# Kernel optimization log

Measured on AMD Instinct MI355X. Metric: run time of the kernel, lower is better.

## Reference

```python
import jax, jax.numpy as jnp
import numpy as np

D_MODEL, D_STATE, B, S = 1024, 64, 8, 2048


def setup_inputs() -> dict:
    key = jax.random.key(0)
    ks = jax.random.split(key, 14)
    inp = {"x": jax.random.normal(ks[0], (B, S, D_MODEL), jnp.float32)}
    names = ["cog", "beh", "env", "delta", "Bp", "Cp"]
    for i, n in enumerate(names):
        inp[f"W_{n}"] = jax.random.normal(ks[1 + 2 * i], (D_STATE, D_MODEL), jnp.float32) / np.sqrt(D_MODEL)
        inp[f"b_{n}"] = jnp.zeros((D_STATE,), jnp.float32)
    # torch init is log(|randn|+1e-4); we use strictly-negative A_log so the
    # length-2048 multiplicative recurrence stays finite (A_log is a learned
    # parameter, so its value is free; the math of forward is unchanged).
    inp["A_log"] = -jnp.abs(jax.random.normal(ks[13], (D_STATE, D_STATE), jnp.float32)) - 0.1
    return inp


def reference(x, W_cog, b_cog, W_beh, b_beh, W_env, b_env,
              W_delta, b_delta, W_Bp, b_Bp, W_Cp, b_Cp, A_log):
    # gating terms (computed in the source but never used downstream)
    A_t = (jax.nn.sigmoid(x @ W_cog.T + b_cog)
           * jax.nn.sigmoid(x @ W_beh.T + b_beh)
           * jax.nn.sigmoid(x @ W_env.T + b_env))
    del A_t

    delta = jax.nn.softplus(x @ W_delta.T + b_delta)   # [B,S,N]
    Bt = x @ W_Bp.T + b_Bp                             # [B,S,N]
    Ct = x @ W_Cp.T + b_Cp                             # [B,S,N]
    u = Bt * x[:, :, :D_STATE]                         # [B,S,N]

    # Faithful to torch broadcasting: after step 0 the carried state h is
    # [B,N,N] with h[b,i,j] = exp(A_log[i,j]*delta[b,t,i]) * h_prev[b,i,j] + u[b,t,j]
    def step(h, td):
        d, u_t, c_t = td                               # each [B,N]
        A = jnp.exp(A_log[None, :, :] * d[:, :, None]) # [B,N,N]
        h = A * h + u_t[:, None, :]
        y = jnp.einsum('bj,bij->bi', c_t, h)           # [B,N]
        return h, y

    h0 = jnp.zeros((x.shape[0], D_STATE, D_STATE), x.dtype)
    _, ys = jax.lax.scan(
        step, h0,
        (delta.transpose(1, 0, 2), u.transpose(1, 0, 2), Ct.transpose(1, 0, 2)))
    # torch stacks y_t of shape [B,1,N] along dim=1 -> [B,S,1,N]
    return ys.transpose(1, 0, 2)[:, :, None, :]
```

## Files before the change

kernel.cpp:

```cpp
#include <hip/hip_runtime.h>
#include <math.h>

#define DM   1024
#define DS   64
#define BATCH 8
#define SEQ  2048
#define CL   32
#define NC   64

typedef __bf16 bf16x8 __attribute__((ext_vector_type(8)));
typedef float  f32x4  __attribute__((ext_vector_type(4)));

#if __has_builtin(__builtin_amdgcn_exp2f)
#define EXP2(v) __builtin_amdgcn_exp2f(v)
#else
#define EXP2(v) __expf(0.69314718056f * (v))
#endif

#define LBAR() do {                                                           \
    asm volatile("s_waitcnt lgkmcnt(0)" ::: "memory");                        \
    __builtin_amdgcn_s_barrier();                                             \
    asm volatile("" ::: "memory");                                            \
} while (0)

__global__ __launch_bounds__(256) void wconv_kernel(
    const float* __restrict__ Wd, const float* __restrict__ Wb,
    const float* __restrict__ Wc, __bf16* __restrict__ Wp)
{
    int idx = blockIdx.x * 256 + threadIdx.x;
    int k  = idx & 1023;
    int n  = idx >> 10;
    const float* W = (n < 64) ? Wd : (n < 128 ? Wb : Wc);
    float v = W[(size_t)(n & 63) * DM + k];
    int kt = k >> 5, kk = k & 31;
    Wp[((size_t)kt * 192 + n) * 32 + kk] = (__bf16)v;
}

__global__ __launch_bounds__(256, 2) void projp1_full(
    const float* __restrict__ x, const __bf16* __restrict__ Wp,
    const float* __restrict__ bd, const float* __restrict__ bb,
    const float* __restrict__ bc, const float* __restrict__ A_log,
    float* __restrict__ delta_g, float* __restrict__ u_g,
    float* __restrict__ ct_g,
    float* __restrict__ E, float* __restrict__ Dsum)
{
    __shared__ __bf16 sA[4][32 * 72];
    __shared__ float  s_d[CL * 64];
    __shared__ float  s_u[CL * 64];

    const int tid  = threadIdx.x;
    const int row0 = blockIdx.x * 32;

    const int lane = tid & 63, wv = tid >> 6;
    const int l15  = lane & 15, quad = lane >> 4;
    const int nbase = wv * 48;

    const int am = tid >> 3;
    const int ak = tid & 7;
    const float* xga = x + (size_t)(row0 + am) * DM + ak * 8;

    const __bf16* wpb = Wp + (nbase + l15) * 32 + quad * 8;

    f32x4 acc[2][3];
    #pragma unroll
    for (int mt = 0; mt < 2; ++mt)
        #pragma unroll
        for (int nt = 0; nt < 3; ++nt)
            acc[mt][nt] = (f32x4){0.f, 0.f, 0.f, 0.f};

    float4 areg[4];
    bf16x8 bA[6], bB[6];

    #define LOADA2(pp) do {                                                   \
        areg[0] = *(const float4*)(xga + (pp) * 128);                         \
        areg[1] = *(const float4*)(xga + (pp) * 128 + 4);                     \
        areg[2] = *(const float4*)(xga + (pp) * 128 + 64);                    \
        areg[3] = *(const float4*)(xga + (pp) * 128 + 68);                    \
    } while (0)
    #define STAGEA2(be, bo) do {                                              \
        bf16x8 h0 = {(__bf16)areg[0].x, (__bf16)areg[0].y,                    \
                     (__bf16)areg[0].z, (__bf16)areg[0].w,                    \
                     (__bf16)areg[1].x, (__bf16)areg[1].y,                    \
                     (__bf16)areg[1].z, (__bf16)areg[1].w};                   \
        *(bf16x8*)&sA[be][am * 72 + ak * 8] = h0;                             \
        bf16x8 h1 = {(__bf16)areg[2].x, (__bf16)areg[2].y,                    \
                     (__bf16)areg[2].z, (__bf16)areg[2].w,                    \
                     (__bf16)areg[3].x, (__bf16)areg[3].y,                    \
                     (__bf16)areg[3].z, (__bf16)areg[3].w};                   \
        *(bf16x8*)&sA[bo][am * 72 + ak * 8] = h1;                             \
    } while (0)
    #define LOADBF(dst, kb) do {                                              \
        const __bf16* wb_ = wpb + (size_t)(kb) * 12288;                       \
        dst[0] = *(const bf16x8*)(wb_);                                       \
        dst[1] = *(const bf16x8*)(wb_ + 512);                                 \
        dst[2] = *(const bf16x8*)(wb_ + 1024);                                \
        dst[3] = *(const bf16x8*)(wb_ + 6144);                                \
        dst[4] = *(const bf16x8*)(wb_ + 6656);                                \
        dst[5] = *(const bf16x8*)(wb_ + 7168);                                \
    } while (0)
    #define COMPUTE(bi, bfr) do {                                             \
        _Pragma("unroll")                                                     \
        for (int s = 0; s < 2; ++s) {                                         \
            bf16x8 af0 = *(const bf16x8*)                                     \
                &sA[bi][(l15) * 72 + s * 32 + quad * 8];                      \
            bf16x8 af1 = *(const bf16x8*)                                     \
                &sA[bi][(16 + l15) * 72 + s * 32 + quad * 8];                 \
            _Pragma("unroll")                                                 \
            for (int nt = 0; nt < 3; ++nt) {                                  \
                acc[0][nt] = __builtin_amdgcn_mfma_f32_16x16x32_bf16(         \
                    af0, bfr[s * 3 + nt], acc[0][nt], 0, 0, 0);               \
                acc[1][nt] = __builtin_amdgcn_mfma_f32_16x16x32_bf16(         \
                    af1, bfr[s * 3 + nt], acc[1][nt], 0, 0, 0);               \
            }                                                                 \
        }                                                                     \
    } while (0)

    LOADA2(0);
    STAGEA2(0, 1);
    LOADA2(1);
    LOADBF(bA, 0);
    LBAR();

    for (int p = 0; p < 8; ++p) {
        const int pe = (p & 1) * 2, po = pe + 1;
        LOADBF(bB, 2 * p + 1);
        COMPUTE(pe, bA);
        if (p < 7) STAGEA2(pe ^ 2, po ^ 2);
        if (p < 6) LOADA2(p + 2);
        if (p < 7) LOADBF(bA, 2 * p + 2);
        COMPUTE(po, bB);
        LBAR();
    }
    #undef LOADA2
    #undef STAGEA2
    #undef LOADBF
    #undef COMPUTE

    #pragma unroll
    for (int nt = 0; nt < 3; ++nt) {
        int gn  = nbase + nt * 16 + l15;
        int mat = (nbase + nt * 16) >> 6;
        int col = gn & 63;
        float bias = (mat == 0) ? bd[col] : (mat == 1 ? bb[col] : bc[col]);
        #pragma unroll
        for (int mt = 0; mt < 2; ++mt) {
            #pragma unroll
            for (int r = 0; r < 4; ++r) {
                int tl = mt * 16 + quad * 4 + r;
                int m  = row0 + tl;
                float v = acc[mt][nt][r] + bias;
                if (mat == 0) {
                    float sp = (v > 20.f) ? v : __logf(1.f + __expf(v));
                    delta_g[(size_t)m * DS + col] = sp;
                    s_d[tl * 64 + col] = sp;
                } else if (mat == 1) {
                    float uu = v * x[(size_t)m * DM + col];
                    u_g[(size_t)m * DS + col] = uu;
                    s_u[tl * 64 + col] = uu;
                } else {
                    ct_g[(size_t)m * DS + col] = v;
                }
            }
        }
    }
    LBAR();

    const int bidx = row0 >> 11;
    const int cidx = (row0 >> 5) & 63;
    const int si = tid & 63;
    const int sj = tid >> 6;

    float alog[16];
    {
        const float4* ar = (const float4*)(A_log + si * 64 + sj * 16);
        #pragma unroll
        for (int qq = 0; qq < 4; ++qq) {
            float4 v = ar[qq];
            alog[4*qq+0] = v.x * 1.44269504f; alog[4*qq+1] = v.y * 1.44269504f;
            alog[4*qq+2] = v.z * 1.44269504f; alog[4*qq+3] = v.w * 1.44269504f;
        }
    }

    float h[16];
    #pragma unroll
    for (int k = 0; k < 16; ++k) h[k] = 0.f;
    float dsum = 0.f;

    #pragma unroll 4
    for (int t = 0; t < CL; ++t) {
        float d = s_d[t * 64 + si];
        dsum += d;
        const float4* up4 = (const float4*)(s_u + t * 64 + sj * 16);
        float4 u0 = up4[0], u1 = up4[1], u2 = up4[2], u3 = up4[3];
        float uv[16] = {u0.x,u0.y,u0.z,u0.w, u1.x,u1.y,u1.z,u1.w,
                        u2.x,u2.y,u2.z,u2.w, u3.x,u3.y,u3.z,u3.w};
        #pragma unroll
        for (int k = 0; k < 16; ++k)
            h[k] = EXP2(alog[k] * d) * h[k] + uv[k];
    }

    float* eo = E + (((size_t)cidx * BATCH + bidx) * 64 + si) * 64 + sj * 16;
    #pragma unroll
    for (int qq = 0; qq < 4; ++qq)
        ((float4*)eo)[qq] = make_float4(h[4*qq], h[4*qq+1], h[4*qq+2], h[4*qq+3]);
    if (sj == 0) Dsum[((size_t)cidx * BATCH + bidx) * 64 + si] = dsum;
}

__device__ __forceinline__ void scan_range8(
    const float* __restrict__ Eb, const float* __restrict__ Db,
    int n0, int n1, int bb_, int i_, int jg_,
    const float* __restrict__ alog, float* __restrict__ h)
{
    if (n0 >= n1) return;
    size_t idx0 = ((size_t)n0 * BATCH + bb_) * 64 + i_;
    float dsA = Db[idx0];
    const float4* ep0 = (const float4*)(Eb + idx0 * 64 + jg_ * 8);
    float4 a0 = ep0[0], a1 = ep0[1];

    float dsB = 0.f;
    float4 b0 = make_float4(0.f,0.f,0.f,0.f), b1 = b0;
    if (n0 + 1 < n1) {
        size_t idx1 = ((size_t)(n0 + 1) * BATCH + bb_) * 64 + i_;
        dsB = Db[idx1];
        const float4* ep1 = (const float4*)(Eb + idx1 * 64 + jg_ * 8);
        b0 = ep1[0]; b1 = ep1[1];
    }

    for (int n = n0; n < n1; ++n) {
        float dsC = 0.f;
        float4 c0 = make_float4(0.f,0.f,0.f,0.f), c1 = c0;
        if (n + 2 < n1) {
            size_t idx2 = ((size_t)(n + 2) * BATCH + bb_) * 64 + i_;
            dsC = Db[idx2];
            const float4* ep2 = (const float4*)(Eb + idx2 * 64 + jg_ * 8);
            c0 = ep2[0]; c1 = ep2[1];
        }
        float ev[8] = {a0.x,a0.y,a0.z,a0.w, a1.x,a1.y,a1.z,a1.w};
        #pragma unroll
        for (int k = 0; k < 8; ++k)
            h[k] = EXP2(alog[k] * dsA) * h[k] + ev[k];
        dsA = dsB; a0 = b0; a1 = b1;
        dsB = dsC; b0 = c0; b1 = c1;
    }
}

__global__ __launch_bounds__(512) void group_kernel(
    const float* __restrict__ E, const float* __restrict__ Dsum,
    const float* __restrict__ A_log,
    float* __restrict__ Eg, float* __restrict__ Dg)
{
    const int g2 = blockIdx.x >> 3, b2 = blockIdx.x & 7;
    const int tid = threadIdx.x;
    const int i  = tid >> 3;
    const int jg = tid & 7;

    float alog[8];
    {
        const float4* ar = (const float4*)(A_log + i * 64 + jg * 8);
        float4 v0 = ar[0], v1 = ar[1];
        alog[0] = v0.x * 1.44269504f; alog[1] = v0.y * 1.44269504f;
        alog[2] = v0.z * 1.44269504f; alog[3] = v0.w * 1.44269504f;
        alog[4] = v1.x * 1.44269504f; alog[5] = v1.y * 1.44269504f;
        alog[6] = v1.z * 1.44269504f; alog[7] = v1.w * 1.44269504f;
    }

    float hg[8];
    #pragma unroll
    for (int k = 0; k < 8; ++k) hg[k] = 0.f;
    scan_range8(E, Dsum, g2 * 8, g2 * 8 + 8, b2, i, jg, alog, hg);

    float4* ego = (float4*)(Eg + (((size_t)g2 * BATCH + b2) * 64 + i) * 64 + jg * 8);
    ego[0] = make_float4(hg[0], hg[1], hg[2], hg[3]);
    ego[1] = make_float4(hg[4], hg[5], hg[6], hg[7]);
    if (jg == 0) {
        float Dacc = 0.f;
        #pragma unroll
        for (int q = 0; q < 8; ++q)
            Dacc += Dsum[((size_t)(g2 * 8 + q) * BATCH + b2) * 64 + i];
        Dg[((size_t)g2 * BATCH + b2) * 64 + i] = Dacc;
    }
}

__global__ __launch_bounds__(512) void pass23_kernel(
    const float* __restrict__ delta_g, const float* __restrict__ u_g,
    const float* __restrict__ ct_g, const float* __restrict__ A_log,
    const float* __restrict__ E, const float* __restrict__ Dsum,
    const float* __restrict__ Eg, const float* __restrict__ Dg,
    float* __restrict__ out)
{
    __shared__ float s_d[CL * 64];
    __shared__ float s_u[CL * 64];
    __shared__ float s_c[CL * 64];

    const int c = blockIdx.x, b = blockIdx.y, tid = threadIdx.x;
    const int t0 = c * CL;

    {
        const float4* dg = (const float4*)(delta_g + ((size_t)b * SEQ + t0) * DS);
        const float4* ug = (const float4*)(u_g     + ((size_t)b * SEQ + t0) * DS);
        const float4* cg = (const float4*)(ct_g    + ((size_t)b * SEQ + t0) * DS);
        ((float4*)s_d)[tid] = dg[tid];
        ((float4*)s_u)[tid] = ug[tid];
        ((float4*)s_c)[tid] = cg[tid];
    }

    const int i  = tid >> 3;
    const int jg = tid & 7;

    float alog[8];
    {
        const float4* ar = (const float4*)(A_log + i * 64 + jg * 8);
        float4 v0 = ar[0], v1 = ar[1];
        alog[0] = v0.x * 1.44269504f; alog[1] = v0.y * 1.44269504f;
        alog[2] = v0.z * 1.44269504f; alog[3] = v0.w * 1.44269504f;
        alog[4] = v1.x * 1.44269504f; alog[5] = v1.y * 1.44269504f;
        alog[6] = v1.z * 1.44269504f; alog[7] = v1.w * 1.44269504f;
    }

    float h[8];
    #pragma unroll
    for (int k = 0; k < 8; ++k) h[k] = 0.f;
    const int g = c >> 3;
    scan_range8(Eg, Dg, 0, g, b, i, jg, alog, h);
    scan_range8(E, Dsum, g * 8, c, b, i, jg, alog, h);
    __syncthreads();

    #pragma unroll 4
    for (int t = 0; t < CL; ++t) {
        float d = s_d[t * 64 + i];
        const float4* up4 = (const float4*)(s_u + t * 64 + jg * 8);
        const float4* cp4 = (const float4*)(s_c + t * 64 + jg * 8);
        float4 u0 = up4[0], u1 = up4[1];
        float4 c0 = cp4[0], c1 = cp4[1];
        float uv[8] = {u0.x,u0.y,u0.z,u0.w, u1.x,u1.y,u1.z,u1.w};
        float cv[8] = {c0.x,c0.y,c0.z,c0.w, c1.x,c1.y,c1.z,c1.w};
        float part = 0.f;
        #pragma unroll
        for (int k = 0; k < 8; ++k) {
            h[k] = EXP2(alog[k] * d) * h[k] + uv[k];
            part += cv[k] * h[k];
        }
        part += __shfl_xor(part, 1);
        part += __shfl_xor(part, 2);
        part += __shfl_xor(part, 4);
        if (jg == 0)
            out[((size_t)b * SEQ + t0 + t) * DS + i] = part;
    }
}

extern "C" void kernel_launch(void* const* d_in, const int* in_sizes, int n_in,
                              void* d_out, int out_size, void* d_ws, size_t ws_size,
                              hipStream_t stream)
{
    (void)in_sizes; (void)n_in; (void)out_size; (void)ws_size;
    const float* x     = (const float*)d_in[0];
    const float* Wd    = (const float*)d_in[7];
    const float* bd    = (const float*)d_in[8];
    const float* Wb    = (const float*)d_in[9];
    const float* bb    = (const float*)d_in[10];
    const float* Wc    = (const float*)d_in[11];
    const float* bc    = (const float*)d_in[12];
    const float* A_log = (const float*)d_in[13];
    float* out = (float*)d_out;

    float* ws = (float*)d_ws;
    float* delta_g = ws;
    float* u_g     = ws + 1 * 1048576;
    float* ct_g    = ws + 2 * 1048576;
    float* E       = ws + 3 * 1048576;
    float* Dsum    = ws + 5242880;
    float* Eg      = ws + 5275648;
    float* Dg      = ws + 5537792;
    __bf16* Wp     = (__bf16*)(ws + 5541888);

    wconv_kernel<<<768, 256, 0, stream>>>(Wd, Wb, Wc, Wp);
    projp1_full<<<512, 256, 0, stream>>>(
        x, Wp, bd, bb, bc, A_log, delta_g, u_g, ct_g, E, Dsum);
    group_kernel<<<64, 512, 0, stream>>>(E, Dsum, A_log, Eg, Dg);
    pass23_kernel<<<dim3(NC, BATCH), 512, 0, stream>>>(
        delta_g, u_g, ct_g, A_log, E, Dsum, Eg, Dg, out);
}
```

Before: 170.3 us.

## Fuse group-level chunk scan into projection kernel via last-block atomic counter

Removes the separate group_kernel launch. Each projp1 block bumps an atomic counter for its (group, batch) pair, and the last of the 8 chunk blocks to arrive computes the group-level combined state Eg and Dg from E and Dsum. This saves a kernel launch and the dependency gap between launches. In exchange it adds a hipMemsetAsync, a threadfence and atomic per block, and a serial scan tail in the last-arriving blocks, each running 256 threads with 16 states per thread. Groups 7 are skipped, as are any not needed by pass23.

New measurement: 260.9 us. +53.2%, slower.

```diff
diff --git a/kernel.cpp b/kernel.cpp
--- a/kernel.cpp
+++ b/kernel.cpp
@@ -36,13 +36,43 @@
     Wp[((size_t)kt * 192 + n) * 32 + kk] = (__bf16)v;
 }
 
+__device__ __forceinline__ void scan_range16(
+    const float* __restrict__ Eb, const float* __restrict__ Db,
+    int n0, int n1, int bb_, int i_, int jg_,
+    const float* __restrict__ alog, float* __restrict__ h)
+{
+    if (n0 >= n1) return;
+    size_t idx = ((size_t)n0 * BATCH + bb_) * 64 + i_;
+    float dsA = Db[idx];
+    const float4* ep = (const float4*)(Eb + idx * 64 + jg_ * 16);
+    float4 e0 = ep[0], e1 = ep[1], e2 = ep[2], e3 = ep[3];
+    for (int n = n0; n < n1; ++n) {
+        float dsN = 0.f;
+        float4 f0 = make_float4(0.f,0.f,0.f,0.f), f1 = f0, f2 = f0, f3 = f0;
+        if (n + 1 < n1) {
+            size_t idx2 = ((size_t)(n + 1) * BATCH + bb_) * 64 + i_;
+            dsN = Db[idx2];
+            const float4* fp = (const float4*)(Eb + idx2 * 64 + jg_ * 16);
+            f0 = fp[0]; f1 = fp[1]; f2 = fp[2]; f3 = fp[3];
+        }
+        float ev[16] = {e0.x,e0.y,e0.z,e0.w, e1.x,e1.y,e1.z,e1.w,
+                        e2.x,e2.y,e2.z,e2.w, e3.x,e3.y,e3.z,e3.w};
+        #pragma unroll
+        for (int k = 0; k < 16; ++k)
+            h[k] = EXP2(alog[k] * dsA) * h[k] + ev[k];
+        dsA = dsN; e0 = f0; e1 = f1; e2 = f2; e3 = f3;
+    }
+}
+
 __global__ __launch_bounds__(256, 2) void projp1_full(
     const float* __restrict__ x, const __bf16* __restrict__ Wp,
     const float* __restrict__ bd, const float* __restrict__ bb,
     const float* __restrict__ bc, const float* __restrict__ A_log,
     float* __restrict__ delta_g, float* __restrict__ u_g,
     float* __restrict__ ct_g,
-    float* __restrict__ E, float* __restrict__ Dsum)
+    float* __restrict__ E, float* __restrict__ Dsum,
+    float* __restrict__ Eg, float* __restrict__ Dg,
+    unsigned* __restrict__ ctrs)
 {
     __shared__ __bf16 sA[4][32 * 72];
     __shared__ float  s_d[CL * 64];
@@ -170,40 +200,82 @@
     const int si = tid & 63;
     const int sj = tid >> 6;
 
-    float alog[16];
     {
+        float alog1[16];
         const float4* ar = (const float4*)(A_log + si * 64 + sj * 16);
         #pragma unroll
         for (int qq = 0; qq < 4; ++qq) {
             float4 v = ar[qq];
-            alog[4*qq+0] = v.x * 1.44269504f; alog[4*qq+1] = v.y * 1.44269504f;
-            alog[4*qq+2] = v.z * 1.44269504f; alog[4*qq+3] = v.w * 1.44269504f;
-        }
-    }
-
-    float h[16];
-    #pragma unroll
-    for (int k = 0; k < 16; ++k) h[k] = 0.f;
-    float dsum = 0.f;
-
-    #pragma unroll 4
-    for (int t = 0; t < CL; ++t) {
-        float d = s_d[t * 64 + si];
-        dsum += d;
-        const float4* up4 = (const float4*)(s_u + t * 64 + sj * 16);
-        float4 u0 = up4[0], u1 = up4[1], u2 = up4[2], u3 = up4[3];
-        float uv[16] = {u0.x,u0.y,u0.z,u0.w, u1.x,u1.y,u1.z,u1.w,
-                        u2.x,u2.y,u2.z,u2.w, u3.x,u3.y,u3.z,u3.w};
-        #pragma unroll
-        for (int k = 0; k < 16; ++k)
-            h[k] = EXP2(alog[k] * d) * h[k] + uv[k];
-    }
-
-    float* eo = E + (((size_t)cidx * BATCH + bidx) * 64 + si) * 64 + sj * 16;
-    #pragma unroll
-    for (int qq = 0; qq < 4; ++qq)
-        ((float4*)eo)[qq] = make_float4(h[4*qq], h[4*qq+1], h[4*qq+2], h[4*qq+3]);
-    if (sj == 0) Dsum[((size_t)cidx * BATCH + bidx) * 64 + si] = dsum;
+            alog1[4*qq+0] = v.x * 1.44269504f; alog1[4*qq+1] = v.y * 1.44269504f;
+            alog1[4*qq+2] = v.z * 1.44269504f; alog1[4*qq+3] = v.w * 1.44269504f;
+        }
+
+        float h[16];
+        #pragma unroll
+        for (int k = 0; k < 16; ++k) h[k] = 0.f;
+        float dsum = 0.f;
+
+        for (int t = 0; t < CL; ++t) {
+            float d = s_d[t * 64 + si];
+            dsum += d;
+            const float* up = s_u + t * 64 + sj * 16;
+            #pragma unroll
+            for (int k = 0; k < 16; ++k)
+                h[k] = EXP2(alog1[k] * d) * h[k] + up[k];
+        }
+
+        float* eo = E + (((size_t)cidx * BATCH + bidx) * 64 + si) * 64 + sj * 16;
+        #pragma unroll
+        for (int qq = 0; qq < 4; ++qq)
+            ((float4*)eo)[qq] =
+                make_float4(h[4*qq], h[4*qq+1], h[4*qq+2], h[4*qq+3]);
+        if (sj == 0) Dsum[((size_t)cidx * BATCH + bidx) * 64 + si] = dsum;
+    }
+
+    const int g2 = cidx >> 3;
+    __threadfence();
+    __syncthreads();
+    if (g2 < 7) {
+        if (tid == 0) {
+            unsigned old = __hip_atomic_fetch_add(
+                &ctrs[g2 * 8 + bidx], 1u, __ATOMIC_ACQ_REL,
+                __HIP_MEMORY_SCOPE_AGENT);
+            ((unsigned*)s_d)[0] = (old == 7u) ? 1u : 0u;
+        }
+        __syncthreads();
+        if (((unsigned*)s_d)[0]) {
+            __threadfence();
+            const int i  = tid >> 2;
+            const int jg = tid & 3;
+            float alogg[16];
+            const float4* ar2 = (const float4*)(A_log + i * 64 + jg * 16);
+            #pragma unroll
+            for (int qq = 0; qq < 4; ++qq) {
+                float4 v = ar2[qq];
+                alogg[4*qq+0] = v.x * 1.44269504f;
+                alogg[4*qq+1] = v.y * 1.44269504f;
+                alogg[4*qq+2] = v.z * 1.44269504f;
+                alogg[4*qq+3] = v.w * 1.44269504f;
+            }
+            float hg[16];
+            #pragma unroll
+            for (int k = 0; k < 16; ++k) hg[k] = 0.f;
+            scan_range16(E, Dsum, g2 * 8, g2 * 8 + 8, bidx, i, jg, alogg, hg);
+            float4* ego = (float4*)(Eg + (((size_t)g2 * BATCH + bidx) * 64 + i)
+                                       * 64 + jg * 16);
+            ego[0] = make_float4(hg[0],  hg[1],  hg[2],  hg[3]);
+            ego[1] = make_float4(hg[4],  hg[5],  hg[6],  hg[7]);
+            ego[2] = make_float4(hg[8],  hg[9],  hg[10], hg[11]);
+            ego[3] = make_float4(hg[12], hg[13], hg[14], hg[15]);
+            if (jg == 0) {
+                float Dacc = 0.f;
+                #pragma unroll
+                for (int q = 0; q < 8; ++q)
+                    Dacc += Dsum[((size_t)(g2 * 8 + q) * BATCH + bidx) * 64 + i];
+                Dg[((size_t)g2 * BATCH + bidx) * 64 + i] = Dacc;
+            }
+        }
+    }
 }
 
 __device__ __forceinline__ void scan_range8(
@@ -241,43 +313,6 @@
             h[k] = EXP2(alog[k] * dsA) * h[k] + ev[k];
         dsA = dsB; a0 = b0; a1 = b1;
         dsB = dsC; b0 = c0; b1 = c1;
-    }
-}
-
-__global__ __launch_bounds__(512) void group_kernel(
-    const float* __restrict__ E, const float* __restrict__ Dsum,
-    const float* __restrict__ A_log,
-    float* __restrict__ Eg, float* __restrict__ Dg)
-{
-    const int g2 = blockIdx.x >> 3, b2 = blockIdx.x & 7;
-    const int tid = threadIdx.x;
-    const int i  = tid >> 3;
-    const int jg = tid & 7;
-
-    float alog[8];
-    {
-        const float4* ar = (const float4*)(A_log + i * 64 + jg * 8);
-        float4 v0 = ar[0], v1 = ar[1];
-        alog[0] = v0.x * 1.44269504f; alog[1] = v0.y * 1.44269504f;
-        alog[2] = v0.z * 1.44269504f; alog[3] = v0.w * 1.44269504f;
-        alog[4] = v1.x * 1.44269504f; alog[5] = v1.y * 1.44269504f;
-        alog[6] = v1.z * 1.44269504f; alog[7] = v1.w * 1.44269504f;
-    }
-
-    float hg[8];
-    #pragma unroll
-    for (int k = 0; k < 8; ++k) hg[k] = 0.f;
-    scan_range8(E, Dsum, g2 * 8, g2 * 8 + 8, b2, i, jg, alog, hg);
-
-    float4* ego = (float4*)(Eg + (((size_t)g2 * BATCH + b2) * 64 + i) * 64 + jg * 8);
-    ego[0] = make_float4(hg[0], hg[1], hg[2], hg[3]);
-    ego[1] = make_float4(hg[4], hg[5], hg[6], hg[7]);
-    if (jg == 0) {
-        float Dacc = 0.f;
-        #pragma unroll
-        for (int q = 0; q < 8; ++q)
-            Dacc += Dsum[((size_t)(g2 * 8 + q) * BATCH + b2) * 64 + i];
-        Dg[((size_t)g2 * BATCH + b2) * 64 + i] = Dacc;
     }
 }
 
@@ -372,11 +407,12 @@
     float* Eg      = ws + 5275648;
     float* Dg      = ws + 5537792;
     __bf16* Wp     = (__bf16*)(ws + 5541888);
-
+    unsigned* ctrs = (unsigned*)(ws + 5640192);
+
+    hipMemsetAsync(ctrs, 0, 64 * sizeof(unsigned), stream);
     wconv_kernel<<<768, 256, 0, stream>>>(Wd, Wb, Wc, Wp);
     projp1_full<<<512, 256, 0, stream>>>(
-        x, Wp, bd, bb, bc, A_log, delta_g, u_g, ct_g, E, Dsum);
-    group_kernel<<<64, 512, 0, stream>>>(E, Dsum, A_log, Eg, Dg);
+        x, Wp, bd, bb, bc, A_log, delta_g, u_g, ct_g, E, Dsum, Eg, Dg, ctrs);
     pass23_kernel<<<dim3(NC, BATCH), 512, 0, stream>>>(
         delta_g, u_g, ct_g, A_log, E, Dsum, Eg, Dg, out);
 }
```
